# Kernel optimization log

Measured on AMD Instinct MI355X. Metric: run time of the kernel, lower is better.

Reference implementation:

```python
import jax, jax.numpy as jnp
import numpy as np

DIM = 512
HID = 2 * DIM          # GAT hidden_feature
LAYERS = 3             # GAT attention_layers
HEADS = 8
HEAD_DIM = DIM // HEADS
SCALE = HEAD_DIM ** -0.5
ALPHA = 0.2            # GAT leaky relu slope


def setup_inputs() -> dict:
    key = jax.random.key(0)
    ks = jax.random.split(key, 16)
    B, N = 8, 1024
    s = lambda shape: 1.0 / np.sqrt(shape[-1])
    return {
        "x": jax.random.normal(ks[0], (B, N, DIM), jnp.float32),
        "adj": jax.random.uniform(ks[1], (B, N, N), jnp.float32),
        "qkv_w": jax.random.normal(ks[2], (3 * DIM, DIM), jnp.float32) * s((3 * DIM, DIM)),
        "proj_w": jax.random.normal(ks[3], (DIM, DIM), jnp.float32) * s((DIM, DIM)),
        "proj_b": jnp.zeros((DIM,), jnp.float32),
        # 3 stacked GraphAttentionLayers (in=DIM -> out=HID)
        "gat_W": jax.random.normal(ks[4], (LAYERS, HID, DIM), jnp.float32) * s((HID, DIM)),
        "gat_Wb": jnp.zeros((LAYERS, HID), jnp.float32),
        "gat_ai": jax.random.normal(ks[5], (LAYERS, HID), jnp.float32) * s((1, HID)),
        "gat_ai_b": jnp.zeros((LAYERS,), jnp.float32),
        "gat_aj": jax.random.normal(ks[6], (LAYERS, HID), jnp.float32) * s((1, HID)),
        "gat_aj_b": jnp.zeros((LAYERS,), jnp.float32),
        # out_attention layer (in=3*HID -> out=DIM), used with return_att=True
        "out_W": jax.random.normal(ks[7], (DIM, LAYERS * HID), jnp.float32) * s((DIM, LAYERS * HID)),
        "out_Wb": jnp.zeros((DIM,), jnp.float32),
        "out_ai": jax.random.normal(ks[8], (DIM,), jnp.float32) * s((1, DIM)),
        "out_ai_b": jnp.zeros((), jnp.float32),
        "out_aj": jax.random.normal(ks[9], (DIM,), jnp.float32) * s((1, DIM)),
        "out_aj_b": jnp.zeros((), jnp.float32),
    }


def _gat(x, adj, gat_W, gat_Wb, gat_ai, gat_ai_b, gat_aj, gat_aj_b,
         out_W, out_Wb, out_ai, out_ai_b, out_aj, out_aj_b):
    # eval mode: all F.dropout calls are identity.
    B, N, _ = x.shape
    # stacked layers: Wh [L,B,N,HID]
    Wh = jnp.einsum("bnc,lhc->lbnh", x, gat_W) + gat_Wb[:, None, None, :]
    e1 = jnp.einsum("lbnh,lh->lbn", Wh, gat_ai) + gat_ai_b[:, None, None]
    e2 = jnp.einsum("lbnh,lh->lbn", Wh, gat_aj) + gat_aj_b[:, None, None]
    e = jax.nn.leaky_relu(e1[..., :, None] + e2[..., None, :], ALPHA)  # [L,B,N,N]
    att = jax.nn.softmax(adj[None] * e, axis=-1)
    h_hat = jax.nn.elu(jnp.einsum("lbnm,lbmh->lbnh", att, Wh))         # [L,B,N,HID]
    h = h_hat.transpose(1, 2, 0, 3).reshape(B, N, LAYERS * HID)        # torch.cat dim=2
    # out_attention with return_att=True
    Who = h @ out_W.T + out_Wb                                          # [B,N,DIM]
    eo1 = Who @ out_ai + out_ai_b                                       # [B,N]
    eo2 = Who @ out_aj + out_aj_b
    eo = jax.nn.leaky_relu(eo1[:, :, None] + eo2[:, None, :], ALPHA)    # [B,N,N]
    att_o = jax.nn.softmax(adj * eo, axis=-1)
    return jax.nn.elu(att_o)


def reference(x, adj, qkv_w, proj_w, proj_b,
              gat_W, gat_Wb, gat_ai, gat_ai_b, gat_aj, gat_aj_b,
              out_W, out_Wb, out_ai, out_ai_b, out_aj, out_aj_b):
    # dataset_name == 'CAD' path
    B, N, C = x.shape
    qkv = (x @ qkv_w.T).reshape(B, N, 3, HEADS, HEAD_DIM).transpose(2, 0, 3, 1, 4)
    q, k, v = qkv[0], qkv[1], qkv[2]                                    # [B,H,N,hd]
    attn = jnp.einsum("bhnd,bhmd->bhnm", q * SCALE, k)                  # [B,H,N,N]
    gmask = _gat(x, adj, gat_W, gat_Wb, gat_ai, gat_ai_b, gat_aj, gat_aj_b,
                 out_W, out_Wb, out_ai, out_ai_b, out_aj, out_aj_b)      # [B,N,N]
    mask = jax.nn.softmax(gmask[:, None, :, :], axis=-1)                # broadcast over heads == repeat
    attn = jax.nn.softmax(mask * attn, axis=-1)
    out = jnp.einsum("bhnm,bhmd->bhnd", attn, v)
    out = out.transpose(0, 2, 1, 3).reshape(B, N, HEADS * HEAD_DIM)
    return out @ proj_w.T + proj_b
```

## Files before the change

### kernel.cpp

```cpp
#include <hip/hip_runtime.h>
#include <math.h>
#include <stdint.h>

#define SCALEQ 0.125f

typedef __bf16 bf16_t;
typedef __bf16 bf16x8 __attribute__((ext_vector_type(8)));
typedef float f32x4 __attribute__((ext_vector_type(4)));

#define GLOAD_LDS16(gsrc, ldst)                                                   \
  __builtin_amdgcn_global_load_lds(                                               \
      (const __attribute__((address_space(1))) void*)(uintptr_t)(const void*)(gsrc), \
      (__attribute__((address_space(3))) void*)(uintptr_t)(void*)(ldst), 16, 0, 0)

__device__ __forceinline__ int3 xswz3() {
  const int nx = gridDim.x, ny = gridDim.y;
  int lin = (blockIdx.z * ny + blockIdx.y) * nx + blockIdx.x;
  const int n = nx * ny * gridDim.z;
  int work = (lin & 7) * (n >> 3) + (lin >> 3);
  int3 r;
  r.x = work % nx; work /= nx;
  r.y = work % ny; r.z = work / ny;
  return r;
}

__device__ __forceinline__ void mm_bf16(const bf16_t* __restrict__ A, int lda,
                                        const bf16_t* __restrict__ B, int ldb,
                                        int K, int m0, int n0,
                                        bf16_t* As, bf16_t* Bs, f32x4 (&acc)[4][4]) {
  const int tid = threadIdx.x, lane = tid & 63, w = tid >> 6;
  const int wr = (w >> 1) * 64, wc = (w & 1) * 64;
  const int fr = lane & 15, fq = lane >> 4;
  const int c8 = (((lane & 7) ^ ((lane >> 3) & 7)) * 8);
  for (int kt = 0; kt < K; kt += 64) {
    __syncthreads();
#pragma unroll
    for (int t = 0; t < 4; ++t) {
      const int rl = t * 32 + w * 8 + (lane >> 3);
      GLOAD_LDS16(A + (size_t)(m0 + rl) * lda + kt + c8, As + (t * 32 + w * 8) * 64);
      GLOAD_LDS16(B + (size_t)(n0 + rl) * ldb + kt + c8, Bs + (t * 32 + w * 8) * 64);
    }
    __syncthreads();
#pragma unroll
    for (int ks = 0; ks < 2; ++ks) {
      bf16x8 af[4], bfv[4];
      const int ch = (((ks * 4 + fq) ^ (fr & 7)) << 3);
#pragma unroll
      for (int mf = 0; mf < 4; ++mf)
        af[mf] = *(const bf16x8*)(As + (wr + mf * 16 + fr) * 64 + ch);
#pragma unroll
      for (int nf = 0; nf < 4; ++nf)
        bfv[nf] = *(const bf16x8*)(Bs + (wc + nf * 16 + fr) * 64 + ch);
#pragma unroll
      for (int mf = 0; mf < 4; ++mf)
#pragma unroll
        for (int nf = 0; nf < 4; ++nf)
          acc[mf][nf] = __builtin_amdgcn_mfma_f32_16x16x32_bf16(af[mf], bfv[nf], acc[mf][nf], 0, 0, 0);
    }
  }
}

#define MM_PROLOGUE()                                  \
  __shared__ __align__(16) bf16_t As[128 * 64];        \
  __shared__ __align__(16) bf16_t Bs[128 * 64];        \
  f32x4 acc[4][4];                                     \
  _Pragma("unroll") for (int i_ = 0; i_ < 4; ++i_)     \
  _Pragma("unroll") for (int j_ = 0; j_ < 4; ++j_) acc[i_][j_] = (f32x4)0.0f;

#define MM_EPI_SETUP(M0, N0)                                   \
  const int lane = threadIdx.x & 63, w = threadIdx.x >> 6;     \
  const int fr = lane & 15, fq = lane >> 4;                    \
  const int mb = (M0) + (w >> 1) * 64, nb = (N0) + (w & 1) * 64;

__global__ __launch_bounds__(256) void k_qkv(const bf16_t* __restrict__ xb, const bf16_t* __restrict__ wb,
                                             bf16_t* __restrict__ qb, bf16_t* __restrict__ kb,
                                             bf16_t* __restrict__ vT) {
  MM_PROLOGUE();
  const int3 bi = xswz3();
  const int m0 = bi.y * 128, n0 = bi.x * 128;
  mm_bf16(xb, 512, wb, 512, 512, m0, n0, As, Bs, acc);
  MM_EPI_SETUP(m0, n0);
#pragma unroll
  for (int mf = 0; mf < 4; ++mf)
#pragma unroll
    for (int nf = 0; nf < 4; ++nf) {
      const int n = nb + nf * 16 + fr;
      const int which = n >> 9, hd = (n >> 6) & 7, d = n & 63;
      const int m_ = mb + mf * 16 + fq * 4;
      const int b = m_ >> 10, tok0 = m_ & 1023;
      if (which == 2) {
        union { ushort4 u; bf16_t q[4]; } pk;
#pragma unroll
        for (int r = 0; r < 4; ++r) pk.q[r] = (bf16_t)acc[mf][nf][r];
        *(ushort4*)(vT + (((size_t)b * 8 + hd) * 64 + d) * 1024 + tok0) = pk.u;
      } else {
        bf16_t* dst = which ? kb : qb;
        const float sc = which ? 1.f : SCALEQ;
#pragma unroll
        for (int r = 0; r < 4; ++r)
          dst[(((size_t)b * 8 + hd) * 1024 + tok0 + r) * 64 + d] = (bf16_t)(acc[mf][nf][r] * sc);
      }
    }
}

__global__ __launch_bounds__(256, 6) void k_wh(const bf16_t* __restrict__ xb, const bf16_t* __restrict__ gatw,
                                               const float* __restrict__ gWb, bf16_t* __restrict__ WhT) {
  MM_PROLOGUE();
  const int3 bi = xswz3();
  const int m0 = bi.y * 128, n0 = bi.x * 128, l = bi.z;
  const bf16_t* Wl = gatw + (size_t)l * 524288;
  const float* Wb = gWb + l * 1024;
  bf16_t* out = WhT + (size_t)l * 8388608;
  mm_bf16(xb, 512, Wl, 512, 512, m0, n0, As, Bs, acc);
  MM_EPI_SETUP(m0, n0);
#pragma unroll
  for (int mf = 0; mf < 4; ++mf)
#pragma unroll
    for (int nf = 0; nf < 4; ++nf) {
      const int h = nb + nf * 16 + fr;
      const float bias = Wb[h];
      const int m_ = mb + mf * 16 + fq * 4;
      const int b = m_ >> 10, ml = m_ & 1023;
      union { ushort4 u; bf16_t q[4]; } pk;
#pragma unroll
      for (int r = 0; r < 4; ++r) pk.q[r] = (bf16_t)(acc[mf][nf][r] + bias);
      *(ushort4*)(out + (((size_t)b << 10) + h) * 1024 + ml) = pk.u;
    }
}

__global__ __launch_bounds__(256, 6) void k_hhat(const bf16_t* __restrict__ att, const bf16_t* __restrict__ WhT,
                                                 bf16_t* __restrict__ hh, int ldh,
                                                 const float* __restrict__ wvo, float* __restrict__ peo) {
  MM_PROLOGUE();
  const int3 bi = xswz3();
  const int m0 = bi.y * 128, n0 = bi.x * 128;
  const int prob = bi.z;
  const int l = prob >> 3, bz = prob & 7;
  const size_t off = ((size_t)prob) << 20;
  mm_bf16(att + off, 1024, WhT + off, 1024, 1024, m0, n0, As, Bs, acc);
  MM_EPI_SETUP(m0, n0);
  if (wvo != nullptr) {
    float w1[4], w2[4];
#pragma unroll
    for (int nf = 0; nf < 4; ++nf) {
      const int n = nb + nf * 16 + fr;
      w1[nf] = wvo[l * 1024 + n];
      w2[nf] = wvo[3072 + l * 1024 + n];
    }
    float* p1 = peo + ((size_t)prob * 8 + bi.x) * 1024;
    float* p2 = p1 + 196608;
#pragma unroll
    for (int mf = 0; mf < 4; ++mf)
#pragma unroll
      for (int r = 0; r < 4; ++r) {
        float s1 = 0.f, s2 = 0.f;
#pragma unroll
        for (int nf = 0; nf < 4; ++nf) {
          float v = acc[mf][nf][r];
          v = v > 0.f ? v : (__expf(v) - 1.f);
          s1 = fmaf(v, w1[nf], s1);
          s2 = fmaf(v, w2[nf], s2);
        }
        s1 += __shfl_xor(s1, 1); s1 += __shfl_xor(s1, 2); s1 += __shfl_xor(s1, 4); s1 += __shfl_xor(s1, 8);
        s2 += __shfl_xor(s2, 1); s2 += __shfl_xor(s2, 2); s2 += __shfl_xor(s2, 4); s2 += __shfl_xor(s2, 8);
        if (fr == 0) {
          const int rowloc = mb + mf * 16 + fq * 4 + r;
          p1[rowloc] = s1;
          p2[rowloc] = s2;
        }
      }
  } else {
#pragma unroll
    for (int mf = 0; mf < 4; ++mf)
#pragma unroll
      for (int nf = 0; nf < 4; ++nf) {
        const int n = nb + nf * 16 + fr;
#pragma unroll
        for (int r = 0; r < 4; ++r) {
          const int m = mb + mf * 16 + fq * 4 + r;
          float v = acc[mf][nf][r];
          v = v > 0.f ? v : (__expf(v) - 1.f);
          hh[(size_t)((bz << 10) + m) * ldh + l * 1024 + n] = (bf16_t)v;
        }
      }
  }
}

__global__ __launch_bounds__(256) void k_eored(const float* __restrict__ peo,
                                               float* __restrict__ eo1, float* __restrict__ eo2) {
  const int m = blockIdx.x * 256 + threadIdx.x;
  const int b = m >> 10, r = m & 1023;
  float s1 = 0.f, s2 = 0.f;
#pragma unroll
  for (int l = 0; l < 3; ++l)
#pragma unroll
    for (int s = 0; s < 8; ++s) {
      const size_t idx = (((size_t)(l * 8 + b)) * 8 + s) * 1024 + r;
      s1 += peo[idx];
      s2 += peo[196608 + idx];
    }
  eo1[m] = s1;
  eo2[m] = s2;
}

__global__ __launch_bounds__(256) void k_lin(const bf16_t* __restrict__ A, int lda,
                                             const bf16_t* __restrict__ B, int K,
                                             const float* __restrict__ bias, float* __restrict__ out) {
  MM_PROLOGUE();
  const int3 bi = xswz3();
  const int m0 = bi.y * 128, n0 = bi.x * 128;
  mm_bf16(A, lda, B, K, K, m0, n0, As, Bs, acc);
  MM_EPI_SETUP(m0, n0);
#pragma unroll
  for (int mf = 0; mf < 4; ++mf)
#pragma unroll
    for (int nf = 0; nf < 4; ++nf) {
      const int n = nb + nf * 16 + fr;
#pragma unroll
      for (int r = 0; r < 4; ++r) {
        const int m = mb + mf * 16 + fq * 4 + r;
        out[(size_t)m * 512 + n] = acc[mf][nf][r] + bias[n];
      }
    }
}

__global__ __launch_bounds__(256) void k_who_acc(const bf16_t* __restrict__ hh, const bf16_t* __restrict__ Wl,
                                                 const float* __restrict__ Wb, float* __restrict__ Who, int l) {
  MM_PROLOGUE();
  const int m0 = blockIdx.y * 128, n0 = blockIdx.x * 128;
  mm_bf16(hh, 1024, Wl, 3072, 1024, m0, n0, As, Bs, acc);
  MM_EPI_SETUP(m0, n0);
#pragma unroll
  for (int mf = 0; mf < 4; ++mf)
#pragma unroll
    for (int nf = 0; nf < 4; ++nf) {
      const int n = nb + nf * 16 + fr;
#pragma unroll
      for (int r = 0; r < 4; ++r) {
        const int m = mb + mf * 16 + fq * 4 + r;
        const size_t idx = (size_t)m * 512 + n;
        Who[idx] = acc[mf][nf][r] + (l == 0 ? Wb[n] : Who[idx]);
      }
    }
}

__global__ __launch_bounds__(256) void k_cast5(const float* __restrict__ s0, bf16_t* __restrict__ d0, int c0,
                                               const float* __restrict__ s1, bf16_t* __restrict__ d1, int c1,
                                               const float* __restrict__ s2, bf16_t* __restrict__ d2, int c2,
                                               const float* __restrict__ s3, bf16_t* __restrict__ d3, int c3,
                                               const float* __restrict__ s4, bf16_t* __restrict__ d4, int c4) {
  int i = blockIdx.x * 256 + threadIdx.x;
  const float* src; bf16_t* dst; int j;
  if (i < c0)      { src = s0; dst = d0; j = i; }
  else if (i < c1) { src = s1; dst = d1; j = i - c0; }
  else if (i < c2) { src = s2; dst = d2; j = i - c1; }
  else if (i < c3) { src = s3; dst = d3; j = i - c2; }
  else if (i < c4) { src = s4; dst = d4; j = i - c3; }
  else return;
  float4 v = ((const float4*)src)[j];
  union { ushort4 u; bf16_t b[4]; } p;
  p.b[0] = (bf16_t)v.x; p.b[1] = (bf16_t)v.y; p.b[2] = (bf16_t)v.z; p.b[3] = (bf16_t)v.w;
  ((ushort4*)dst)[j] = p.u;
}

__global__ __launch_bounds__(256) void k_wvec(const bf16_t* __restrict__ gatwb,
                                              const float* __restrict__ gWb,
                                              const float* __restrict__ ai, const float* __restrict__ aib,
                                              const float* __restrict__ aj, const float* __restrict__ ajb,
                                              float* __restrict__ wv, float* __restrict__ con) {
  __shared__ float sred[4][64];
  __shared__ float cred[256];
  const int v = blockIdx.y, l = v >> 1;
  const float* avec = ((v & 1) ? aj : ai) + (l << 10);
  const bf16_t* W = gatwb + ((size_t)(l << 10)) * 512;
  const int tid = threadIdx.x, hg = tid >> 6, cc = tid & 63;
  const int c = blockIdx.x * 64 + cc;
  float p = 0.f;
  for (int i = 0; i < 256; ++i) {
    const int h = hg * 256 + i;
    p = fmaf((float)W[(size_t)h * 512 + c], avec[h], p);
  }
  sred[hg][cc] = p;
  float cp = 0.f;
#pragma unroll
  for (int i = 0; i < 4; ++i) cp = fmaf(gWb[(l << 10) + tid + i * 256], avec[tid + i * 256], cp);
  cred[tid] = cp;
  __syncthreads();
  if (tid < 64) wv[v * 512 + blockIdx.x * 64 + tid] = sred[0][tid] + sred[1][tid] + sred[2][tid] + sred[3][tid];
  for (int s = 128; s > 0; s >>= 1) {
    if (tid < s) cred[tid] += cred[tid + s];
    __syncthreads();
  }
  if (tid == 0 && blockIdx.x == 0) con[v] = cred[0] + ((v & 1) ? ajb[l] : aib[l]);
}

__global__ __launch_bounds__(256) void k_wvec_o(const float* __restrict__ W, const float* __restrict__ Wb,
                                                const float* __restrict__ ai, const float* __restrict__ aj,
                                                float* __restrict__ wvo, float* __restrict__ conO) {
  const int c = blockIdx.x * 256 + threadIdx.x;
  const int d0 = blockIdx.y * 64;
  float s1 = 0.f, s2 = 0.f;
  for (int t = 0; t < 64; ++t) {
    const float w = W[(size_t)(d0 + t) * 3072 + c];
    s1 = fmaf(w, ai[d0 + t], s1);
    s2 = fmaf(w, aj[d0 + t], s2);
  }
  atomicAdd(&wvo[c], s1);
  atomicAdd(&wvo[3072 + c], s2);
  if (blockIdx.x == 0 && threadIdx.x < 64) {
    const int d = d0 + threadIdx.x;
    float c1 = Wb[d] * ai[d], c2 = Wb[d] * aj[d];
#pragma unroll
    for (int off = 32; off > 0; off >>= 1) { c1 += __shfl_xor(c1, off); c2 += __shfl_xor(c2, off); }
    if (threadIdx.x == 0) { atomicAdd(&conO[0], c1); atomicAdd(&conO[1], c2); }
  }
}

__global__ __launch_bounds__(256) void k_e12v(const bf16_t* __restrict__ xb,
                                              const float* __restrict__ wv, const float* __restrict__ con,
                                              float* __restrict__ ev) {
  const int tid = threadIdx.x, lane = tid & 63, wid = tid >> 6;
  const int row = blockIdx.x * 4 + wid;
  bf16x8 xv = *(const bf16x8*)(xb + (size_t)row * 512 + lane * 8);
  float xf[8];
#pragma unroll
  for (int j = 0; j < 8; ++j) xf[j] = (float)xv[j];
  float s[6];
#pragma unroll
  for (int v = 0; v < 6; ++v) {
    const float* wp = wv + v * 512 + lane * 8;
    float a = 0.f;
#pragma unroll
    for (int j = 0; j < 8; ++j) a = fmaf(xf[j], wp[j], a);
    s[v] = a;
  }
#pragma unroll
  for (int v = 0; v < 6; ++v)
#pragma unroll
    for (int off = 32; off > 0; off >>= 1) s[v] += __shfl_xor(s[v], off);
  if (lane == 0) {
#pragma unroll
    for (int v = 0; v < 6; ++v) ev[v * 8192 + row] = s[v] + con[v];
  }
}

__global__ __launch_bounds__(256) void k_eo(const float* __restrict__ Who,
                                            const float* __restrict__ ai, const float* __restrict__ aj,
                                            float* __restrict__ eo1, float* __restrict__ eo2) {
  const int wid = threadIdx.x >> 6, lane = threadIdx.x & 63;
  const int row = blockIdx.x * 4 + wid;
  const float* wr = Who + (size_t)row * 512;
  float s1 = 0.f, s2 = 0.f;
#pragma unroll
  for (int c = 0; c < 2; ++c) {
    const int idx = c * 256 + lane * 4;
    float4 w4 = *(const float4*)&wr[idx];
    float4 a4 = *(const float4*)&ai[idx];
    float4 b4 = *(const float4*)&aj[idx];
    s1 += w4.x * a4.x + w4.y * a4.y + w4.z * a4.z + w4.w * a4.w;
    s2 += w4.x * b4.x + w4.y * b4.y + w4.z * b4.z + w4.w * b4.w;
  }
#pragma unroll
  for (int off = 32; off > 0; off >>= 1) { s1 += __shfl_xor(s1, off); s2 += __shfl_xor(s2, off); }
  if (lane == 0) { eo1[row] = s1; eo2[row] = s2; }
}

__device__ __forceinline__ float block_max(float v, float* red) {
#pragma unroll
  for (int off = 32; off > 0; off >>= 1) v = fmaxf(v, __shfl_xor(v, off));
  __syncthreads();
  if ((threadIdx.x & 63) == 0) red[threadIdx.x >> 6] = v;
  __syncthreads();
  return fmaxf(fmaxf(red[0], red[1]), fmaxf(red[2], red[3]));
}
__device__ __forceinline__ float block_sum(float v, float* red) {
#pragma unroll
  for (int off = 32; off > 0; off >>= 1) v += __shfl_xor(v, off);
  __syncthreads();
  if ((threadIdx.x & 63) == 0) red[threadIdx.x >> 6] = v;
  __syncthreads();
  return red[0] + red[1] + red[2] + red[3];
}

__global__ __launch_bounds__(256) void k_gat_att3(const float* __restrict__ adj, const float* __restrict__ ev,
                                                  bf16_t* __restrict__ att) {
  const int lane = threadIdx.x & 63;
  const int row = blockIdx.x * 4 + (threadIdx.x >> 6);
  const int b = row >> 10;
  const float* arow = adj + (size_t)row * 1024;
  float a[4][4];
#pragma unroll
  for (int c = 0; c < 4; ++c) *(float4*)a[c] = *(const float4*)&arow[(c * 64 + lane) * 4];
#pragma unroll
  for (int l = 0; l < 3; ++l) {
    const float e1v = ev[l * 16384 + row];
    const float* e2r = ev + l * 16384 + 8192 + (b << 10);
    bf16_t* aout = att + (size_t)l * 8388608 + (size_t)row * 1024;
    float s[4][4];
    float mx = -1e30f;
#pragma unroll
    for (int c = 0; c < 4; ++c) {
      float4 e4 = *(const float4*)&e2r[(c * 64 + lane) * 4];
      float ee[4] = {e4.x, e4.y, e4.z, e4.w};
#pragma unroll
      for (int j = 0; j < 4; ++j) {
        float e = e1v + ee[j];
        e = e > 0.f ? e : 0.2f * e;
        s[c][j] = a[c][j] * e;
        mx = fmaxf(mx, s[c][j]);
      }
    }
#pragma unroll
    for (int off = 32; off > 0; off >>= 1) mx = fmaxf(mx, __shfl_xor(mx, off));
    float sum = 0.f;
#pragma unroll
    for (int c = 0; c < 4; ++c)
#pragma unroll
      for (int j = 0; j < 4; ++j) { float p = __expf(s[c][j] - mx); s[c][j] = p; sum += p; }
#pragma unroll
    for (int off = 32; off > 0; off >>= 1) sum += __shfl_xor(sum, off);
    const float inv = 1.f / sum;
#pragma unroll
    for (int c = 0; c < 4; ++c) {
      union { ushort4 u; bf16_t q[4]; } pk;
#pragma unroll
      for (int j = 0; j < 4; ++j) pk.q[j] = (bf16_t)(s[c][j] * inv);
      *(ushort4*)(aout + (c * 64 + lane) * 4) = pk.u;
    }
  }
}

__global__ __launch_bounds__(256) void k_gat_att(const float* __restrict__ adj, const float* __restrict__ ev,
                                                 bf16_t* __restrict__ att) {
  __shared__ float red[4];
  const int row = blockIdx.x;
  const int b = row >> 10;
  const float* arow = adj + (size_t)row * 1024;
  const float e1v = ev[row];
  const float* e2r = ev + 8192 + (b << 10);
  float s[4];
  float mx = -1e30f;
#pragma unroll
  for (int c = 0; c < 4; ++c) {
    const int m = c * 256 + threadIdx.x;
    float e = e1v + e2r[m];
    e = e > 0.f ? e : 0.2f * e;
    s[c] = arow[m] * e;
    mx = fmaxf(mx, s[c]);
  }
  mx = block_max(mx, red);
  float sum = 0.f;
#pragma unroll
  for (int c = 0; c < 4; ++c) { float p = __expf(s[c] - mx); s[c] = p; sum += p; }
  sum = block_sum(sum, red);
  const float inv = 1.f / sum;
#pragma unroll
  for (int c = 0; c < 4; ++c) att[(size_t)row * 1024 + c * 256 + threadIdx.x] = (bf16_t)(s[c] * inv);
}

__global__ __launch_bounds__(256) void k_mask(const float* __restrict__ adj, const float* __restrict__ eo1,
                                              const float* __restrict__ eo2, const float* __restrict__ conO,
                                              const float* __restrict__ aib, const float* __restrict__ ajb,
                                              bf16_t* __restrict__ mask) {
  const int lane = threadIdx.x & 63;
  const int row = blockIdx.x * 4 + (threadIdx.x >> 6);
  const int b = row >> 10;
  const float* arow = adj + (size_t)row * 1024;
  const float t1 = eo1[row] + conO[0] + aib[0];
  const float c2 = conO[1] + ajb[0];
  const float* eor = eo2 + (b << 10);
  float s[4][4];
  float mx = -1e30f;
#pragma unroll
  for (int c = 0; c < 4; ++c) {
    float4 a4 = *(const float4*)&arow[(c * 64 + lane) * 4];
    float4 e4 = *(const float4*)&eor[(c * 64 + lane) * 4];
    float aa[4] = {a4.x, a4.y, a4.z, a4.w};
    float ee[4] = {e4.x, e4.y, e4.z, e4.w};
#pragma unroll
    for (int j = 0; j < 4; ++j) {
      float e = t1 + ee[j] + c2;
      e = e > 0.f ? e : 0.2f * e;
      s[c][j] = aa[j] * e;
      mx = fmaxf(mx, s[c][j]);
    }
  }
#pragma unroll
  for (int off = 32; off > 0; off >>= 1) mx = fmaxf(mx, __shfl_xor(mx, off));
  float sum = 0.f;
#pragma unroll
  for (int c = 0; c < 4; ++c)
#pragma unroll
    for (int j = 0; j < 4; ++j) { float p = __expf(s[c][j] - mx); s[c][j] = p; sum += p; }
#pragma unroll
  for (int off = 32; off > 0; off >>= 1) sum += __shfl_xor(sum, off);
  const float inv = 1.f / sum;
  float sum2 = 0.f;
#pragma unroll
  for (int c = 0; c < 4; ++c)
#pragma unroll
    for (int j = 0; j < 4; ++j) { float p = __expf(s[c][j] * inv - inv); s[c][j] = p; sum2 += p; }
#pragma unroll
  for (int off = 32; off > 0; off >>= 1) sum2 += __shfl_xor(sum2, off);
  const float inv2 = 1.f / sum2;
#pragma unroll
  for (int c = 0; c < 4; ++c) {
    union { ushort4 u; bf16_t q[4]; } pk;
#pragma unroll
    for (int j = 0; j < 4; ++j) pk.q[j] = (bf16_t)(s[c][j] * inv2);
    *(ushort4*)(mask + (size_t)row * 1024 + (c * 64 + lane) * 4) = pk.u;
  }
}

__global__ __launch_bounds__(256) void k_mtr(const bf16_t* __restrict__ in, bf16_t* __restrict__ out) {
  __shared__ bf16_t T[64][72];
  const int q0 = blockIdx.x * 64, k0 = blockIdx.y * 64, b = blockIdx.z;
  const bf16_t* src = in + ((size_t)b << 20);
  bf16_t* dst = out + ((size_t)b << 20);
  const int r = threadIdx.x >> 2, c = (threadIdx.x & 3) * 16;
  bf16x8 a0 = *(const bf16x8*)(src + (size_t)(q0 + r) * 1024 + k0 + c);
  bf16x8 a1 = *(const bf16x8*)(src + (size_t)(q0 + r) * 1024 + k0 + c + 8);
  *(bf16x8*)&T[r][c] = a0;
  *(bf16x8*)&T[r][c + 8] = a1;
  __syncthreads();
  union { bf16x8 v[2]; bf16_t e[16]; } o;
#pragma unroll
  for (int j = 0; j < 16; ++j) o.e[j] = T[c + j][r];
  *(bf16x8*)(dst + (size_t)(k0 + r) * 1024 + q0 + c) = o.v[0];
  *(bf16x8*)(dst + (size_t)(k0 + r) * 1024 + q0 + c + 8) = o.v[1];
}

__device__ __forceinline__ int swz(int row, int slot) { return row * 64 + ((slot ^ (row & 7)) << 3); }

__global__ __launch_bounds__(256) void k_flash(const bf16_t* __restrict__ qg, const bf16_t* __restrict__ kg,
                                               const bf16_t* __restrict__ vTg, const bf16_t* __restrict__ maskT,
                                               bf16_t* __restrict__ aout) {
  __shared__ __align__(16) bf16_t Ks[4096];
  __shared__ __align__(16) bf16_t Vs[4096];
  __shared__ __align__(16) bf16_t PL[4][1024];
  const int tid = threadIdx.x, lane = tid & 63, w = tid >> 6;
  const int fr = lane & 15, fq = lane >> 4;
  const int3 bi = xswz3();
  const int n0 = bi.x * 64, hh = bi.y, bb = bi.z;
  const size_t bh = ((size_t)bb * 8 + hh) << 16;
  const bf16_t* q = qg + bh;
  const bf16_t* kk = kg + bh;
  const bf16_t* vT = vTg + bh;
  const bf16_t* mT = maskT + ((size_t)bb << 20);
  bf16_t* PLw = &PL[w][0];

  bf16x8 qf[2];
#pragma unroll
  for (int ks = 0; ks < 2; ++ks)
    qf[ks] = *(const bf16x8*)(q + (size_t)(n0 + w * 16 + fr) * 64 + ks * 32 + fq * 8);

  f32x4 o[4];
#pragma unroll
  for (int nf = 0; nf < 4; ++nf) o[nf] = (f32x4)0.0f;
  float psum[4] = {0.f, 0.f, 0.f, 0.f};

  const int srow = tid >> 2, sslot = (tid & 3) * 2;
  const int ws0 = swz(srow, sslot), ws1 = swz(srow, sslot + 1);
  const int scol = (tid & 3) * 16;

  for (int c = 0; c < 16; ++c) {
    const int k0 = c * 64;
    bf16x8 kv0 = *(const bf16x8*)(kk + (size_t)(k0 + srow) * 64 + scol);
    bf16x8 kv1 = *(const bf16x8*)(kk + (size_t)(k0 + srow) * 64 + scol + 8);
    bf16x8 vv0 = *(const bf16x8*)(vT + (size_t)srow * 1024 + k0 + scol);
    bf16x8 vv1 = *(const bf16x8*)(vT + (size_t)srow * 1024 + k0 + scol + 8);
    union { ushort4 u; bf16_t h[4]; } mfr[4];
#pragma unroll
    for (int nf = 0; nf < 4; ++nf)
      mfr[nf].u = *(const ushort4*)(mT + (size_t)(k0 + nf * 16 + fr) * 1024 + n0 + w * 16 + fq * 4);
    __syncthreads();
    *(bf16x8*)&Ks[ws0] = kv0; *(bf16x8*)&Ks[ws1] = kv1;
    *(bf16x8*)&Vs[ws0] = vv0; *(bf16x8*)&Vs[ws1] = vv1;
    __syncthreads();

    f32x4 s[4];
#pragma unroll
    for (int nf = 0; nf < 4; ++nf) s[nf] = (f32x4)0.0f;
#pragma unroll
    for (int ks = 0; ks < 2; ++ks) {
      bf16x8 kf[4];
#pragma unroll
      for (int nf = 0; nf < 4; ++nf)
        kf[nf] = *(const bf16x8*)&Ks[swz(nf * 16 + fr, ks * 4 + fq)];
#pragma unroll
      for (int nf = 0; nf < 4; ++nf)
        s[nf] = __builtin_amdgcn_mfma_f32_16x16x32_bf16(qf[ks], kf[nf], s[nf], 0, 0, 0);
    }

#pragma unroll
    for (int nf = 0; nf < 4; ++nf)
#pragma unroll
      for (int r = 0; r < 4; ++r) {
        const float p = __expf(s[nf][r] * (float)mfr[nf].h[r]);
        psum[r] += p;
        const int pp = fq * 4 + r, e = nf * 16 + fr;
        PLw[pp * 64 + ((((e >> 3) ^ (pp & 7))) << 3) + (e & 7)] = (bf16_t)p;
      }

#pragma unroll
    for (int ks = 0; ks < 2; ++ks) {
      bf16x8 pf = *(const bf16x8*)&PLw[swz(fr, ks * 4 + fq)];
      bf16x8 vf[4];
#pragma unroll
      for (int nfo = 0; nfo < 4; ++nfo)
        vf[nfo] = *(const bf16x8*)&Vs[swz(nfo * 16 + fr, ks * 4 + fq)];
#pragma unroll
      for (int nfo = 0; nfo < 4; ++nfo)
        o[nfo] = __builtin_amdgcn_mfma_f32_16x16x32_bf16(pf, vf[nfo], o[nfo], 0, 0, 0);
    }
  }

#pragma unroll
  for (int r = 0; r < 4; ++r) {
    psum[r] += __shfl_xor(psum[r], 1);
    psum[r] += __shfl_xor(psum[r], 2);
    psum[r] += __shfl_xor(psum[r], 4);
    psum[r] += __shfl_xor(psum[r], 8);
  }
#pragma unroll
  for (int r = 0; r < 4; ++r) {
    const int tok = n0 + w * 16 + fq * 4 + r;
    const float inv = 1.f / psum[r];
#pragma unroll
    for (int nfo = 0; nfo < 4; ++nfo)
      aout[((size_t)(bb << 10) + tok) * 512 + hh * 64 + nfo * 16 + fr] = (bf16_t)(o[nfo][r] * inv);
  }
}

extern "C" void kernel_launch(void* const* d_in, const int* in_sizes, int n_in,
                              void* d_out, int out_size, void* d_ws, size_t ws_size,
                              hipStream_t stream) {
  (void)in_sizes; (void)n_in; (void)out_size;
  const float* x        = (const float*)d_in[0];
  const float* adj      = (const float*)d_in[1];
  const float* qkv_w    = (const float*)d_in[2];
  const float* proj_w   = (const float*)d_in[3];
  const float* proj_b   = (const float*)d_in[4];
  const float* gat_W    = (const float*)d_in[5];
  const float* gat_Wb   = (const float*)d_in[6];
  const float* gat_ai   = (const float*)d_in[7];
  const float* gat_ai_b = (const float*)d_in[8];
  const float* gat_aj   = (const float*)d_in[9];
  const float* gat_aj_b = (const float*)d_in[10];
  const float* out_W    = (const float*)d_in[11];
  const float* out_Wb   = (const float*)d_in[12];
  const float* out_ai   = (const float*)d_in[13];
  const float* out_ai_b = (const float*)d_in[14];
  const float* out_aj   = (const float*)d_in[15];
  const float* out_aj_b = (const float*)d_in[16];

  char* p = (char*)d_ws;
  auto alloc = [&](size_t bytes) { char* r = p; p += (bytes + 255) & ~(size_t)255; return r; };
  bf16_t* xb     = (bf16_t*)alloc(8192ull * 512 * 2);
  bf16_t* qkvwb  = (bf16_t*)alloc(1536ull * 512 * 2);
  bf16_t* gatwb  = (bf16_t*)alloc(3072ull * 512 * 2);
  bf16_t* outwb  = (bf16_t*)alloc(512ull * 3072 * 2);
  bf16_t* projwb = (bf16_t*)alloc(512ull * 512 * 2);
  bf16_t* qb     = (bf16_t*)alloc(8ull * 8 * 1024 * 64 * 2);
  bf16_t* kb     = (bf16_t*)alloc(8ull * 8 * 1024 * 64 * 2);
  bf16_t* vT     = (bf16_t*)alloc(8ull * 8 * 64 * 1024 * 2);
  float*  Who    = (float*)alloc(8192ull * 512 * 4);
  float*  wv     = (float*)alloc(6 * 512 * 4);
  float*  con    = (float*)alloc(256);
  float*  ev     = (float*)alloc(6 * 8192 * 4);
  float*  eo1    = (float*)alloc(8192 * 4);
  float*  eo2    = (float*)alloc(8192 * 4);
  float*  peo    = (float*)alloc(2ull * 196608 * 4);
  float*  wvo    = (float*)alloc(2 * 3072 * 4);
  float*  conO   = (float*)alloc(256);
  const size_t zspan = (size_t)((char*)conO - (char*)wvo) + 256;

  const bool big = ws_size >= 211000000ull;

  const dim3 blk(256);
  k_cast5<<<8192, blk, 0, stream>>>(x, xb, 1048576, qkv_w, qkvwb, 1245184, gat_W, gatwb, 1638400,
                                    out_W, outwb, 2031616, proj_w, projwb, 2097152);
  hipMemsetAsync(wvo, 0, zspan, stream);
  k_wvec<<<dim3(8, 6), blk, 0, stream>>>(gatwb, gat_Wb, gat_ai, gat_ai_b, gat_aj, gat_aj_b, wv, con);
  k_wvec_o<<<dim3(12, 8), blk, 0, stream>>>(out_W, out_Wb, out_ai, out_aj, wvo, conO);
  k_e12v<<<2048, blk, 0, stream>>>(xb, wv, con, ev);
  k_qkv<<<dim3(12, 64), blk, 0, stream>>>(xb, qkvwb, qb, kb, vT);

  if (big) {
    bf16_t* WhT3 = (bf16_t*)alloc(3ull * 8 * 1024 * 1024 * 2);
    bf16_t* att3 = (bf16_t*)alloc(3ull * 8 * 1024 * 1024 * 2);
    bf16_t* mask  = att3;
    bf16_t* maskT = att3 + 8388608;
    bf16_t* aoutb = att3 + 2 * 8388608;

    k_wh<<<dim3(8, 64, 3), blk, 0, stream>>>(xb, gatwb, gat_Wb, WhT3);
    k_gat_att3<<<2048, blk, 0, stream>>>(adj, ev, att3);
    k_hhat<<<dim3(8, 8, 24), blk, 0, stream>>>(att3, WhT3, (bf16_t*)Who, 3072, wvo, peo);
    k_eored<<<32, blk, 0, stream>>>(peo, eo1, eo2);
    k_mask<<<2048, blk, 0, stream>>>(adj, eo1, eo2, conO, out_ai_b, out_aj_b, mask);
    k_mtr<<<dim3(16, 16, 8), blk, 0, stream>>>(mask, maskT);
    k_flash<<<dim3(16, 8, 8), blk, 0, stream>>>(qb, kb, vT, maskT, aoutb);
    k_lin<<<dim3(4, 64), blk, 0, stream>>>(aoutb, 512, projwb, 512, proj_b, (float*)d_out);
  } else {
    bf16_t* WhT   = (bf16_t*)alloc(8ull * 1024 * 1024 * 2);
    bf16_t* att   = (bf16_t*)alloc(8ull * 1024 * 1024 * 2);
    bf16_t* hh    = (bf16_t*)alloc(8192ull * 1024 * 2);
    bf16_t* aoutb = (bf16_t*)alloc(8192ull * 512 * 2);
    bf16_t* maskT = (bf16_t*)alloc(8ull * 1024 * 1024 * 2);
    bf16_t* mask  = att;

    for (int l = 0; l < 3; ++l) {
      k_wh<<<dim3(8, 64, 1), blk, 0, stream>>>(xb, gatwb + (size_t)l * 524288, gat_Wb + l * 1024, WhT);
      k_gat_att<<<8192, blk, 0, stream>>>(adj, ev + (size_t)l * 16384, att);
      k_hhat<<<dim3(8, 8, 8), blk, 0, stream>>>(att, WhT, hh, 1024, nullptr, nullptr);
      k_who_acc<<<dim3(4, 64), blk, 0, stream>>>(hh, outwb + l * 1024, out_Wb, Who, l);
    }
    k_eo<<<2048, blk, 0, stream>>>(Who, out_ai, out_aj, eo1, eo2);
    k_mask<<<2048, blk, 0, stream>>>(adj, eo1, eo2, conO, out_ai_b, out_aj_b, mask);
    k_mtr<<<dim3(16, 16, 8), blk, 0, stream>>>(mask, maskT);
    k_flash<<<dim3(16, 8, 8), blk, 0, stream>>>(qb, kb, vT, maskT, aoutb);
    k_lin<<<dim3(4, 64), blk, 0, stream>>>(aoutb, 512, projwb, 512, proj_b, (float*)d_out);
  }
}
```

Before: 281.1 us.

## Add 256x256-tile 512-thread batched GEMM for fused GAT hhat path

```diff
diff --git a/kernel.cpp b/kernel.cpp
--- a/kernel.cpp
+++ b/kernel.cpp
@@ -103,8 +103,8 @@
     }
 }
 
-__global__ __launch_bounds__(256, 6) void k_wh(const bf16_t* __restrict__ xb, const bf16_t* __restrict__ gatw,
-                                               const float* __restrict__ gWb, bf16_t* __restrict__ WhT) {
+__global__ __launch_bounds__(256) void k_wh(const bf16_t* __restrict__ xb, const bf16_t* __restrict__ gatw,
+                                            const float* __restrict__ gWb, bf16_t* __restrict__ WhT) {
   MM_PROLOGUE();
   const int3 bi = xswz3();
   const int m0 = bi.y * 128, n0 = bi.x * 128, l = bi.z;
@@ -128,9 +128,103 @@
     }
 }
 
-__global__ __launch_bounds__(256, 6) void k_hhat(const bf16_t* __restrict__ att, const bf16_t* __restrict__ WhT,
-                                                 bf16_t* __restrict__ hh, int ldh,
+__global__ __launch_bounds__(512) void k_hhat256(const bf16_t* __restrict__ att, const bf16_t* __restrict__ WhT,
                                                  const float* __restrict__ wvo, float* __restrict__ peo) {
+  __shared__ __align__(16) bf16_t LA[2][256 * 64];
+  __shared__ __align__(16) bf16_t LB[2][256 * 64];
+  const int tid = threadIdx.x, lane = tid & 63, w = tid >> 6;
+  const int fr = lane & 15, fq = lane >> 4;
+  const int3 bi = xswz3();
+  const int prob = bi.z, l = prob >> 3;
+  const size_t off = ((size_t)prob) << 20;
+  const bf16_t* A = att + off;
+  const bf16_t* B = WhT + off;
+  const int m0 = bi.y * 256, n0 = bi.x * 256;
+  const int srow = w * 32 + (lane >> 3);
+  const int c8 = (((lane & 7) ^ ((lane >> 3) & 7)) * 8);
+
+  f32x4 acc[8][4];
+#pragma unroll
+  for (int mf = 0; mf < 8; ++mf)
+#pragma unroll
+    for (int nf = 0; nf < 4; ++nf) acc[mf][nf] = (f32x4)0.0f;
+
+  {
+    const int kofs = c8;
+#pragma unroll
+    for (int t = 0; t < 4; ++t) {
+      const int r = srow + t * 8;
+      GLOAD_LDS16(A + (size_t)(m0 + r) * 1024 + kofs, &LA[0][(w * 32 + t * 8) * 64]);
+      GLOAD_LDS16(B + (size_t)(n0 + r) * 1024 + kofs, &LB[0][(w * 32 + t * 8) * 64]);
+    }
+  }
+  __syncthreads();
+
+  const int wrow = (w >> 2) * 128, wcol = (w & 3) * 64;
+  for (int t = 0; t < 16; ++t) {
+    const int cur = t & 1;
+    if (t < 15) {
+      const int kofs = (t + 1) * 64 + c8;
+#pragma unroll
+      for (int u = 0; u < 4; ++u) {
+        const int r = srow + u * 8;
+        GLOAD_LDS16(A + (size_t)(m0 + r) * 1024 + kofs, &LA[cur ^ 1][(w * 32 + u * 8) * 64]);
+        GLOAD_LDS16(B + (size_t)(n0 + r) * 1024 + kofs, &LB[cur ^ 1][(w * 32 + u * 8) * 64]);
+      }
+    }
+    const bf16_t* la = &LA[cur][0];
+    const bf16_t* lb = &LB[cur][0];
+#pragma unroll
+    for (int ks = 0; ks < 2; ++ks) {
+      const int ch = (((ks * 4 + fq) ^ (fr & 7)) << 3);
+      bf16x8 bfv[4];
+#pragma unroll
+      for (int nf = 0; nf < 4; ++nf)
+        bfv[nf] = *(const bf16x8*)(lb + (wcol + nf * 16 + fr) * 64 + ch);
+#pragma unroll
+      for (int mf = 0; mf < 8; ++mf) {
+        bf16x8 af = *(const bf16x8*)(la + (wrow + mf * 16 + fr) * 64 + ch);
+#pragma unroll
+        for (int nf = 0; nf < 4; ++nf)
+          acc[mf][nf] = __builtin_amdgcn_mfma_f32_16x16x32_bf16(af, bfv[nf], acc[mf][nf], 0, 0, 0);
+      }
+    }
+    __syncthreads();
+  }
+
+  float w1[4], w2[4];
+#pragma unroll
+  for (int nf = 0; nf < 4; ++nf) {
+    const int n = n0 + wcol + nf * 16 + fr;
+    w1[nf] = wvo[l * 1024 + n];
+    w2[nf] = wvo[3072 + l * 1024 + n];
+  }
+  float* p1 = peo + (((size_t)prob * 16) + bi.x * 4 + (w & 3)) * 1024;
+  float* p2 = p1 + 393216;
+#pragma unroll
+  for (int mf = 0; mf < 8; ++mf)
+#pragma unroll
+    for (int r = 0; r < 4; ++r) {
+      float s1 = 0.f, s2 = 0.f;
+#pragma unroll
+      for (int nf = 0; nf < 4; ++nf) {
+        float v = acc[mf][nf][r];
+        v = v > 0.f ? v : (__expf(v) - 1.f);
+        s1 = fmaf(v, w1[nf], s1);
+        s2 = fmaf(v, w2[nf], s2);
+      }
+      s1 += __shfl_xor(s1, 1); s1 += __shfl_xor(s1, 2); s1 += __shfl_xor(s1, 4); s1 += __shfl_xor(s1, 8);
+      s2 += __shfl_xor(s2, 1); s2 += __shfl_xor(s2, 2); s2 += __shfl_xor(s2, 4); s2 += __shfl_xor(s2, 8);
+      if (fr == 0) {
+        const int rowloc = m0 + wrow + mf * 16 + fq * 4 + r;
+        p1[rowloc] = s1;
+        p2[rowloc] = s2;
+      }
+    }
+}
+
+__global__ __launch_bounds__(256) void k_hhat(const bf16_t* __restrict__ att, const bf16_t* __restrict__ WhT,
+                                              bf16_t* __restrict__ hh, int ldh) {
   MM_PROLOGUE();
   const int3 bi = xswz3();
   const int m0 = bi.y * 128, n0 = bi.x * 128;
@@ -139,51 +233,19 @@
   const size_t off = ((size_t)prob) << 20;
   mm_bf16(att + off, 1024, WhT + off, 1024, 1024, m0, n0, As, Bs, acc);
   MM_EPI_SETUP(m0, n0);
-  if (wvo != nullptr) {
-    float w1[4], w2[4];
+#pragma unroll
+  for (int mf = 0; mf < 4; ++mf)
 #pragma unroll
     for (int nf = 0; nf < 4; ++nf) {
       const int n = nb + nf * 16 + fr;
-      w1[nf] = wvo[l * 1024 + n];
-      w2[nf] = wvo[3072 + l * 1024 + n];
-    }
-    float* p1 = peo + ((size_t)prob * 8 + bi.x) * 1024;
-    float* p2 = p1 + 196608;
-#pragma unroll
-    for (int mf = 0; mf < 4; ++mf)
 #pragma unroll
       for (int r = 0; r < 4; ++r) {
-        float s1 = 0.f, s2 = 0.f;
-#pragma unroll
-        for (int nf = 0; nf < 4; ++nf) {
-          float v = acc[mf][nf][r];
-          v = v > 0.f ? v : (__expf(v) - 1.f);
-          s1 = fmaf(v, w1[nf], s1);
-          s2 = fmaf(v, w2[nf], s2);
-        }
-        s1 += __shfl_xor(s1, 1); s1 += __shfl_xor(s1, 2); s1 += __shfl_xor(s1, 4); s1 += __shfl_xor(s1, 8);
-        s2 += __shfl_xor(s2, 1); s2 += __shfl_xor(s2, 2); s2 += __shfl_xor(s2, 4); s2 += __shfl_xor(s2, 8);
-        if (fr == 0) {
-          const int rowloc = mb + mf * 16 + fq * 4 + r;
-          p1[rowloc] = s1;
-          p2[rowloc] = s2;
-        }
-      }
-  } else {
-#pragma unroll
-    for (int mf = 0; mf < 4; ++mf)
-#pragma unroll
-      for (int nf = 0; nf < 4; ++nf) {
-        const int n = nb + nf * 16 + fr;
-#pragma unroll
-        for (int r = 0; r < 4; ++r) {
-          const int m = mb + mf * 16 + fq * 4 + r;
-          float v = acc[mf][nf][r];
-          v = v > 0.f ? v : (__expf(v) - 1.f);
-          hh[(size_t)((bz << 10) + m) * ldh + l * 1024 + n] = (bf16_t)v;
-        }
-      }
-  }
+        const int m = mb + mf * 16 + fq * 4 + r;
+        float v = acc[mf][nf][r];
+        v = v > 0.f ? v : (__expf(v) - 1.f);
+        hh[(size_t)((bz << 10) + m) * ldh + l * 1024 + n] = (bf16_t)v;
+      }
+    }
 }
 
 __global__ __launch_bounds__(256) void k_eored(const float* __restrict__ peo,
@@ -194,10 +256,10 @@
 #pragma unroll
   for (int l = 0; l < 3; ++l)
 #pragma unroll
-    for (int s = 0; s < 8; ++s) {
-      const size_t idx = (((size_t)(l * 8 + b)) * 8 + s) * 1024 + r;
+    for (int s = 0; s < 16; ++s) {
+      const size_t idx = (((size_t)(l * 8 + b)) * 16 + s) * 1024 + r;
       s1 += peo[idx];
-      s2 += peo[196608 + idx];
+      s2 += peo[393216 + idx];
     }
   eo1[m] = s1;
   eo2[m] = s2;
@@ -670,7 +732,7 @@
   float*  ev     = (float*)alloc(6 * 8192 * 4);
   float*  eo1    = (float*)alloc(8192 * 4);
   float*  eo2    = (float*)alloc(8192 * 4);
-  float*  peo    = (float*)alloc(2ull * 196608 * 4);
+  float*  peo    = (float*)alloc(2ull * 393216 * 4);
   float*  wvo    = (float*)alloc(2 * 3072 * 4);
   float*  conO   = (float*)alloc(256);
   const size_t zspan = (size_t)((char*)conO - (char*)wvo) + 256;
@@ -695,7 +757,7 @@
 
     k_wh<<<dim3(8, 64, 3), blk, 0, stream>>>(xb, gatwb, gat_Wb, WhT3);
     k_gat_att3<<<2048, blk, 0, stream>>>(adj, ev, att3);
-    k_hhat<<<dim3(8, 8, 24), blk, 0, stream>>>(att3, WhT3, (bf16_t*)Who, 3072, wvo, peo);
+    k_hhat256<<<dim3(4, 4, 24), dim3(512), 0, stream>>>(att3, WhT3, wvo, peo);
     k_eored<<<32, blk, 0, stream>>>(peo, eo1, eo2);
     k_mask<<<2048, blk, 0, stream>>>(adj, eo1, eo2, conO, out_ai_b, out_aj_b, mask);
     k_mtr<<<dim3(16, 16, 8), blk, 0, stream>>>(mask, maskT);
@@ -712,7 +774,7 @@
     for (int l = 0; l < 3; ++l) {
       k_wh<<<dim3(8, 64, 1), blk, 0, stream>>>(xb, gatwb + (size_t)l * 524288, gat_Wb + l * 1024, WhT);
       k_gat_att<<<8192, blk, 0, stream>>>(adj, ev + (size_t)l * 16384, att);
-      k_hhat<<<dim3(8, 8, 8), blk, 0, stream>>>(att, WhT, hh, 1024, nullptr, nullptr);
+      k_hhat<<<dim3(8, 8, 8), blk, 0, stream>>>(att, WhT, hh, 1024);
       k_who_acc<<<dim3(4, 64), blk, 0, stream>>>(hh, outwb + l * 1024, out_Wb, Who, l);
     }
     k_eo<<<2048, blk, 0, stream>>>(Who, out_ai, out_aj, eo1, eo2);
```

Result: faster. 274.4 us (-2.4%).
